# Kernel tuning notes

Hardware: AMD Instinct MI355X
Metric: run time of the kernel (lower is better)

The kernel has to match this reference:

```python
import jax, jax.numpy as jnp
import numpy as np

# hypercfg constants (init_kwargs)
AUX = 0.05
L1W = 5.0
VPW = 1.0
VNW = 1.0


def _lsa_square(cost):
    """Jonker-Volgenant shortest-augmenting-path Hungarian on a square numpy
    cost matrix. Returns rows[j] = row assigned to column j. Runs on host,
    mirroring the original CPU scipy.optimize.linear_sum_assignment call."""
    n = cost.shape[0]
    INF = np.inf
    u = np.zeros(n + 1)
    v = np.zeros(n + 1)
    p = np.zeros(n + 1, dtype=np.int64)   # p[j] = row matched to column j (1-indexed)
    way = np.zeros(n + 1, dtype=np.int64)
    for i in range(1, n + 1):
        p[0] = i
        j0 = 0
        minv = np.full(n + 1, INF)
        used = np.zeros(n + 1, dtype=bool)
        while True:
            used[j0] = True
            i0 = p[j0]
            cur = cost[i0 - 1, :] - u[i0] - v[1:]
            free = ~used[1:]
            upd = free & (cur < minv[1:])
            minv1 = minv[1:]
            minv1[upd] = cur[upd]
            way1 = way[1:]
            way1[upd] = j0
            mfree = np.where(free, minv1, INF)
            j1 = int(np.argmin(mfree)) + 1
            delta = mfree[j1 - 1]
            used_idx = np.nonzero(used)[0]
            u[p[used_idx]] += delta
            v[used_idx] -= delta
            minv1[free] -= delta
            j0 = j1
            if p[j0] == 0:
                break
        while j0 != 0:
            j1 = way[j0]
            p[j0] = p[j1]
            j0 = j1
    return p[1:] - 1


def _match(cost_mk):
    """Rectangular assignment, cost [M, K] with K <= M: pad with a constant
    column block (dummy columns cost the same for any row, so the real K
    columns get the optimal assignment, matching scipy on rectangles)."""
    M, K = cost_mk.shape
    pad = np.zeros((M, M), dtype=np.float64)
    pad[:, :K] = cost_mk
    rows = _lsa_square(pad)
    return rows[:K]


def _cost(meta_points, meta_visibles, gtpoints, gtvisibles):
    # meta_points: [S,B,L,M,2]  gtpoints: [S,B,K,2]
    # meta_visibles: [S,B,M,1]  gtvisibles: [S,B,K,1]
    S, B, L, M, _ = meta_points.shape
    # pairwise L1 cost: [S,B,L,M,K]
    diff = jnp.abs(meta_points[:, :, :, :, None, :] - gtpoints[:, :, None, None, :, :]).sum(-1)
    # delta[l] = L - (l+1), per-layer slack (torch.linspace(1, L, L))
    delta = (L - jnp.arange(1, L + 1, dtype=meta_points.dtype)) * AUX
    cost_p_ml = jax.nn.relu(diff - delta[None, None, :, None, None])
    gtv = gtvisibles[:, :, :, 0][:, :, None, :]          # [S,B,1,K]
    cost_p = gtv * cost_p_ml.mean(2)                     # [S,B,M,K]
    cost_vp = -gtv * jnp.log(meta_visibles)              # [S,B,M,1] -> [S,B,M,K]
    cost_vn = -(1.0 - gtv) * jnp.log(1.0 - meta_visibles)
    cost = L1W * cost_p + VPW * cost_vp + VNW * cost_vn  # [S,B,M,K]
    return cost.mean(0)                                  # mean over shots -> [B,M,K]


def setup_inputs() -> dict:
    key = jax.random.key(0)
    ks = jax.random.split(key, 5)
    S, B, L, M, K = 6, 16, 8, 256, 128
    meta_points = jax.random.uniform(ks[0], (S, B, L, M, 2), dtype=jnp.float32)
    # keep probabilities strictly inside (0,1) so log() is finite
    meta_visibles = jax.random.uniform(ks[1], (S, B, M, 1), dtype=jnp.float32) * 0.9 + 0.05
    covisibles = jax.random.uniform(ks[2], (B, K), dtype=jnp.float32)
    gtpoints = jax.random.uniform(ks[3], (S, B, K, 2), dtype=jnp.float32)
    gtvisibles = (jax.random.uniform(ks[4], (S, B, K, 1)) > 0.5).astype(jnp.float32)
    return {
        "meta_points": meta_points,
        "meta_visibles": meta_visibles,
        "covisibles": covisibles,
        "gtpoints": gtpoints,
        "gtvisibles": gtvisibles,
    }


def reference(meta_points, meta_visibles, covisibles, gtpoints, gtvisibles):
    # covisibles only provides the batch size in the original module
    cost = np.asarray(jax.jit(_cost)(meta_points, meta_visibles, gtpoints, gtvisibles))
    bs = cost.shape[0]
    # per-batch Hungarian on host (sequential data-dependent algorithm);
    # result[b, k] = meta index matched to keypoint k (already kp-sorted,
    # matching the argsort-reorder in the torch code)
    out = np.stack([_match(cost[b]) for b in range(bs)])
    return jnp.asarray(out, dtype=jnp.int64)
```

## Files before the change

kernel.cpp:

```cpp
#include <hip/hip_runtime.h>
#include <math.h>


#define S_ 6
#define B_ 16
#define L_ 8
#define M_ 256
#define K_ 128

__global__ void cost_kernel(const float* __restrict__ mp,
                            const float* __restrict__ mv,
                            const float* __restrict__ gt,
                            const float* __restrict__ gv,
                            float* __restrict__ cost)
{
#pragma clang fp contract(off)
    const int b = blockIdx.x;
    const int m = blockIdx.y;
    const int k = threadIdx.x;

    float accS = 0.0f;
    for (int s = 0; s < S_; ++s) {
        const int sb = s * B_ + b;
        const float gx = gt[(sb * K_ + k) * 2 + 0];
        const float gy = gt[(sb * K_ + k) * 2 + 1];
        float accL = 0.0f;
#pragma unroll
        for (int l = 0; l < L_; ++l) {
            const int base = ((sb * L_ + l) * M_ + m) * 2;
            const float dx = fabsf(mp[base + 0] - gx);
            const float dy = fabsf(mp[base + 1] - gy);
            const float diff = dx + dy;
            const float dl = (float)(L_ - (l + 1)) * 0.05f;
            const float t = diff - dl;
            accL += fmaxf(t, 0.0f);
        }
        const float meanL = accL * 0.125f;
        const float mvv = mv[sb * M_ + m];
        const float gtv = gv[sb * K_ + k];
        const float lp = -logf(mvv);
        const float ln = -logf(1.0f - mvv);
        const float val = (gtv != 0.0f) ? (5.0f * meanL + lp) : ln;
        accS += val;
    }
    cost[(b * M_ + m) * K_ + k] = accS * (1.0f / 6.0f);
}

__device__ __forceinline__ double bits2d(int lo, int hi) {
    const unsigned long long u =
        ((unsigned long long)(unsigned)hi << 32) | (unsigned)lo;
    return __longlong_as_double((long long)u);
}
__device__ __forceinline__ void d2bits(double d, int& lo, int& hi) {
    const unsigned long long u = (unsigned long long)__double_as_longlong(d);
    lo = (int)(u & 0xffffffffull);
    hi = (int)(u >> 32);
}
__device__ __forceinline__ unsigned long long vkey_desc(double v) {
    const double c = v + 0.0;
    const unsigned long long bts = (unsigned long long)__double_as_longlong(c);
    const unsigned long long mask =
        (unsigned long long)((long long)bts >> 63) | 0x8000000000000000ull;
    return ~(bts ^ mask);
}

__global__ __launch_bounds__(64, 1) void match_kernel(const float* __restrict__ cost,
                                                      int* __restrict__ out)
{
#pragma clang fp contract(off)
    const int b = blockIdx.x;
    const int lane = threadIdx.x;
    const float* C = cost + (size_t)b * M_ * K_;
    const double INF = __builtin_inf();
    const int BIG = 0x7fffffff;

    __shared__ float   C_lds[M_ * K_];
    __shared__ double  u_lds[257];
    __shared__ int     p_lds[257];
    __shared__ double  vd_lds[128];
    __shared__ double2 vurec[130];
    __shared__ int     jrec[130];
    __shared__ double  Dcons[128];

    for (int t = lane; t < (M_ * K_) / 4; t += 64)
        ((float4*)C_lds)[t] = ((const float4*)C)[t];

    for (int t = lane; t < 257; t += 64) {
        u_lds[t] = 0.0;
        p_lds[t] = (t >= 129) ? (t - 128) : 0;
    }
    for (int t = lane; t < 128; t += 64) vd_lds[t] = 0.0;
    __syncthreads();

    double v0 = 0.0, v1 = 0.0;

    for (int i = 129; i <= 256; ++i) {
        const int pj0 = p_lds[2 * lane + 1];
        const int pj1 = p_lds[2 * lane + 2];
        float2 cc = *(const float2*)(C_lds + (i - 1) * K_ + 2 * lane);
        const double up0 = u_lds[pj0], up1 = u_lds[pj1];
        double ur0 = up0, ur1 = up1;

        unsigned long long ks0 = vkey_desc(vd_lds[2 * lane]);
        unsigned long long ks1 = vkey_desc(vd_lds[2 * lane + 1]);
        int js0 = 2 * lane + 129;
        int js1 = 2 * lane + 130;
        for (int k = 2; k <= 128; k <<= 1) {
            const bool asc = ((lane & (k >> 1)) == 0);
            for (int d2 = k >> 1; d2 >= 1; d2 >>= 1) {
                if (d2 == 1) {
                    const bool L = (ks0 < ks1) || (ks0 == ks1 && js0 < js1);
                    if (L != asc) {
                        const unsigned long long tk = ks0; ks0 = ks1; ks1 = tk;
                        const int tj = js0; js0 = js1; js1 = tj;
                    }
                } else {
                    const int d = d2 >> 1;
                    const unsigned long long pk0 = __shfl_xor(ks0, d);
                    const int pj0s = __shfl_xor(js0, d);
                    const unsigned long long pk1 = __shfl_xor(ks1, d);
                    const int pj1s = __shfl_xor(js1, d);
                    const bool lower = ((lane & d) == 0);
                    const bool L0 = (ks0 < pk0) || (ks0 == pk0 && js0 < pj0s);
                    const bool L1 = (ks1 < pk1) || (ks1 == pk1 && js1 < pj1s);
                    const bool keep0 = (lower == asc) ? L0 : !L0;
                    const bool keep1 = (lower == asc) ? L1 : !L1;
                    if (!keep0) { ks0 = pk0; js0 = pj0s; }
                    if (!keep1) { ks1 = pk1; js1 = pj1s; }
                }
            }
        }
        jrec[2 * lane] = js0;
        jrec[2 * lane + 1] = js1;
        vurec[2 * lane]     = make_double2(vd_lds[js0 - 129], u_lds[js0 - 128]);
        vurec[2 * lane + 1] = make_double2(vd_lds[js1 - 129], u_lds[js1 - 128]);
        if (lane == 0) { vurec[128] = make_double2(-INF, 0.0); jrec[128] = 257; }
        __syncthreads();

        double2 vuC = vurec[0]; int jdC = jrec[0];
        double2 vuN = vurec[1]; int jdN = jrec[1];
        int ptr = 0;

        int used = 0;
        double u_i0 = 0.0;
        double usum = 0.0;
        int j1 = 0;

        for (;;) {
            const float2 ccs = *(const float2*)(C_lds + (jdC - 129) * K_ + 2 * lane);
            const double dval = (0.0 - u_i0) - vuC.x;

            double cd0 = ((double)cc.x - u_i0) - v0;
            double cd1 = ((double)cc.y - u_i0) - v1;
            if (used & 1) cd0 = INF;
            if (used & 2) cd1 = INF;
            double bv = fmin(cd0, cd1);

            int lo, hi; d2bits(bv, lo, hi);
#define MIN_STAGE(CTRL, RM)                                                      \
            {                                                                    \
                const int nlo = __builtin_amdgcn_update_dpp(lo, lo, CTRL, RM, 0xf, false); \
                const int nhi = __builtin_amdgcn_update_dpp(hi, hi, CTRL, RM, 0xf, false); \
                const double mv2 = fmin(bits2d(lo, hi), bits2d(nlo, nhi));       \
                d2bits(mv2, lo, hi);                                             \
            }
            MIN_STAGE(0x111, 0xf)
            MIN_STAGE(0x112, 0xf)
            MIN_STAGE(0x114, 0xf)
            MIN_STAGE(0x118, 0xf)
            MIN_STAGE(0x142, 0xa)
            MIN_STAGE(0x143, 0xc)
#undef MIN_STAGE
            const int mlo = __builtin_amdgcn_readlane(lo, 63);
            const int mhi = __builtin_amdgcn_readlane(hi, 63);
            const double rmin = bits2d(mlo, mhi);

            if (rmin <= dval) {
                const double delta = rmin;
                usum += delta;
                if (used & 1) { ur0 += delta; v0 -= delta; }
                if (used & 2) { ur1 += delta; v1 -= delta; }

                int jr = BIG;
                if (cd1 == delta) jr = 2 * lane + 2;
                if (cd0 == delta) jr = 2 * lane + 1;
                const unsigned long long br = __ballot(jr != BIG);
                j1 = __builtin_amdgcn_readlane(jr, (int)__builtin_ctzll(br));

                const int ol = (j1 - 1) >> 1, sl = (j1 - 1) & 1;
                const int psel = sl ? pj1 : pj0;
                const int i0n = __builtin_amdgcn_readlane(psel, ol);
                if (i0n == 0) break;

                const double usel = sl ? up1 : up0;
                int ulo, uhi; d2bits(usel, ulo, uhi);
                const double u_n = bits2d(__builtin_amdgcn_readlane(ulo, ol),
                                          __builtin_amdgcn_readlane(uhi, ol));
                if (lane == ol) used |= (1 << sl);
                u_i0 = u_n;
                cc = *(const float2*)(C_lds + (i0n - 1) * K_ + 2 * lane);
            } else {
                const double delta = dval;
                usum += delta;
                if (used & 1) { ur0 += delta; v0 -= delta; }
                if (used & 2) { ur1 += delta; v1 -= delta; }
                if (lane == 0) Dcons[ptr] = usum;
                u_i0 = vuC.y;
                cc = ccs;
                vuC = vuN; jdC = jdN;
                ++ptr;
                vuN = vurec[ptr + 1]; jdN = jrec[ptr + 1];
            }
        }

        __syncthreads();
        if (used & 1) u_lds[pj0] = ur0;
        if (used & 2) u_lds[pj1] = ur1;
        {
            const int t0i = 2 * lane, t1i = 2 * lane + 1;
            if (t0i < ptr) {
                const double amt = usum - Dcons[t0i];
                u_lds[js0 - 128] += amt;
                vd_lds[js0 - 129] -= amt;
            }
            if (t1i < ptr) {
                const double amt = usum - Dcons[t1i];
                u_lds[js1 - 128] += amt;
                vd_lds[js1 - 129] -= amt;
            }
        }
        if (lane == 0) { p_lds[j1] = i; u_lds[i] = usum; }
        __syncthreads();
    }

    for (int j = lane; j < K_; j += 64)
        out[b * K_ + j] = p_lds[j + 1] - 1;
}

extern "C" void kernel_launch(void* const* d_in, const int* in_sizes, int n_in,
                              void* d_out, int out_size, void* d_ws, size_t ws_size,
                              hipStream_t stream) {
    const float* mp = (const float*)d_in[0];
    const float* mv = (const float*)d_in[1];
    const float* gt = (const float*)d_in[3];
    const float* gv = (const float*)d_in[4];
    int* out = (int*)d_out;
    float* cost = (float*)d_ws;

    dim3 gridA(B_, M_);
    cost_kernel<<<gridA, K_, 0, stream>>>(mp, mv, gt, gv, cost);
    match_kernel<<<B_, 64, 0, stream>>>(cost, out);
}
```

Measured before the change: 1.558 ms.

## Cache per-dummy-row column minima and skip runs of dummy-row steps in Hungarian

```diff
diff --git a/kernel.cpp b/kernel.cpp
--- a/kernel.cpp
+++ b/kernel.cpp
@@ -56,6 +56,11 @@
     lo = (int)(u & 0xffffffffull);
     hi = (int)(u >> 32);
 }
+__device__ __forceinline__ double readlane_d(double d, int l) {
+    int lo, hi; d2bits(d, lo, hi);
+    return bits2d(__builtin_amdgcn_readlane(lo, l),
+                  __builtin_amdgcn_readlane(hi, l));
+}
 __device__ __forceinline__ unsigned long long vkey_desc(double v) {
     const double c = v + 0.0;
     const unsigned long long bts = (unsigned long long)__double_as_longlong(c);
@@ -63,6 +68,60 @@
         (unsigned long long)((long long)bts >> 63) | 0x8000000000000000ull;
     return ~(bts ^ mask);
 }
+
+#define RSTG(LOV, HIV, FOP, CTRL, RM)                                            \
+    {                                                                            \
+        const int nlo_ = __builtin_amdgcn_update_dpp(LOV, LOV, CTRL, RM, 0xf, false); \
+        const int nhi_ = __builtin_amdgcn_update_dpp(HIV, HIV, CTRL, RM, 0xf, false); \
+        const double r_ = FOP(bits2d(LOV, HIV), bits2d(nlo_, nhi_));             \
+        d2bits(r_, LOV, HIV);                                                    \
+    }
+#define RLADDER(LOV, HIV, FOP)                                                   \
+    RSTG(LOV, HIV, FOP, 0x111, 0xf)                              \
+    RSTG(LOV, HIV, FOP, 0x112, 0xf)                              \
+    RSTG(LOV, HIV, FOP, 0x114, 0xf)                              \
+    RSTG(LOV, HIV, FOP, 0x118, 0xf)                              \
+    RSTG(LOV, HIV, FOP, 0x142, 0xa)                \
+    RSTG(LOV, HIV, FOP, 0x143, 0xc)
+
+#define FREEMIN(R0B, CMV, CJV)                                                   \
+    {                                                                            \
+        double cd0_ = (double)C_lds[(R0B) * K_ + 2 * lane] - v0;                 \
+        double cd1_ = (double)C_lds[(R0B) * K_ + 2 * lane + 1] - v1;             \
+        if (used & 1) cd0_ = INF;                                                \
+        if (used & 2) cd1_ = INF;                                                \
+        double bv_ = fmin(cd0_, cd1_);                                           \
+        int lo_, hi_; d2bits(bv_, lo_, hi_);                                     \
+        RLADDER(lo_, hi_, fmin)                                                  \
+        CMV = bits2d(__builtin_amdgcn_readlane(lo_, 63),                         \
+                     __builtin_amdgcn_readlane(hi_, 63));                        \
+        int jr_ = BIG;                                                           \
+        if (cd1_ == CMV) jr_ = 2 * lane + 2;                                     \
+        if (cd0_ == CMV) jr_ = 2 * lane + 1;                                     \
+        const unsigned long long br_ = __ballot(jr_ != BIG);                     \
+        CJV = __builtin_amdgcn_readlane(jr_, (int)__builtin_ctzll(br_));         \
+    }
+
+#define SWEEP()                                                                  \
+    {                                                                            \
+        for (int g_ = 0; g_ < 2; ++g_) {                                         \
+            const int R_ = 64 * g_ + lane;                                       \
+            double bm_ = INF; int bc_ = BIG;                                     \
+            for (int it_ = 0; it_ < 128; ++it_) {                                \
+                const int c_ = (it_ + lane) & 127;                               \
+                const double cd_ = (double)C_lds[R_ * K_ + c_] - v_tab[c_];      \
+                if (cd_ < bm_ || (cd_ == bm_ && c_ + 1 < bc_)) {                 \
+                    bm_ = cd_; bc_ = c_ + 1;                                     \
+                }                                                                \
+            }                                                                    \
+            cmin_lds[R_] = bm_; cjmin_lds[R_] = bc_;                             \
+        }                                                                        \
+    }
+
+#define SVREAD(T) readlane_d((((T) & 1) ? sv1 : sv0), (T) >> 1)
+#define SUREAD(T) readlane_d((((T) & 1) ? su1 : su0), (T) >> 1)
+#define DDREAD(T) readlane_d((((T) & 1) ? dd1 : dd0), (T) >> 1)
+#define JSREAD(T) __builtin_amdgcn_readlane(((((T) & 1)) ? js1 : js0), (T) >> 1)
 
 __global__ __launch_bounds__(64, 1) void match_kernel(const float* __restrict__ cost,
                                                       int* __restrict__ out)
@@ -72,24 +131,30 @@
     const int lane = threadIdx.x;
     const float* C = cost + (size_t)b * M_ * K_;
     const double INF = __builtin_inf();
+    const double NINF = -__builtin_inf();
     const int BIG = 0x7fffffff;
 
-    __shared__ float   C_lds[M_ * K_];
-    __shared__ double  u_lds[257];
-    __shared__ int     p_lds[257];
-    __shared__ double  vd_lds[128];
-    __shared__ double2 vurec[130];
-    __shared__ int     jrec[130];
-    __shared__ double  Dcons[128];
+    __shared__ float  C_lds[M_ * K_];
+    __shared__ double u_lds[257];
+    __shared__ int    p_lds[257];
+    __shared__ double vd_lds[128];
+    __shared__ double v_tab[128];
+    __shared__ double cmin_lds[128];
+    __shared__ int    cjmin_lds[128];
+    __shared__ double Sul[128];
+    __shared__ int    Sjl[128];
+    __shared__ double Dcons[128];
 
     for (int t = lane; t < (M_ * K_) / 4; t += 64)
         ((float4*)C_lds)[t] = ((const float4*)C)[t];
-
     for (int t = lane; t < 257; t += 64) {
         u_lds[t] = 0.0;
         p_lds[t] = (t >= 129) ? (t - 128) : 0;
     }
-    for (int t = lane; t < 128; t += 64) vd_lds[t] = 0.0;
+    for (int t = lane; t < 128; t += 64) { vd_lds[t] = 0.0; v_tab[t] = 0.0; }
+    __syncthreads();
+
+    SWEEP()
     __syncthreads();
 
     double v0 = 0.0, v1 = 0.0;
@@ -97,9 +162,7 @@
     for (int i = 129; i <= 256; ++i) {
         const int pj0 = p_lds[2 * lane + 1];
         const int pj1 = p_lds[2 * lane + 2];
-        float2 cc = *(const float2*)(C_lds + (i - 1) * K_ + 2 * lane);
         const double up0 = u_lds[pj0], up1 = u_lds[pj1];
-        double ur0 = up0, ur1 = up1;
 
         unsigned long long ks0 = vkey_desc(vd_lds[2 * lane]);
         unsigned long long ks1 = vkey_desc(vd_lds[2 * lane + 1]);
@@ -109,8 +172,8 @@
             const bool asc = ((lane & (k >> 1)) == 0);
             for (int d2 = k >> 1; d2 >= 1; d2 >>= 1) {
                 if (d2 == 1) {
-                    const bool L = (ks0 < ks1) || (ks0 == ks1 && js0 < js1);
-                    if (L != asc) {
+                    const bool Lc = (ks0 < ks1) || (ks0 == ks1 && js0 < js1);
+                    if (Lc != asc) {
                         const unsigned long long tk = ks0; ks0 = ks1; ks1 = tk;
                         const int tj = js0; js0 = js1; js1 = tj;
                     }
@@ -130,107 +193,120 @@
                 }
             }
         }
-        jrec[2 * lane] = js0;
-        jrec[2 * lane + 1] = js1;
-        vurec[2 * lane]     = make_double2(vd_lds[js0 - 129], u_lds[js0 - 128]);
-        vurec[2 * lane + 1] = make_double2(vd_lds[js1 - 129], u_lds[js1 - 128]);
-        if (lane == 0) { vurec[128] = make_double2(-INF, 0.0); jrec[128] = 257; }
+        const double sv0 = vd_lds[js0 - 129], sv1 = vd_lds[js1 - 129];
+        const double su0 = u_lds[js0 - 128],  su1 = u_lds[js1 - 128];
+        Sul[2 * lane] = su0; Sul[2 * lane + 1] = su1;
+        Sjl[2 * lane] = js0; Sjl[2 * lane + 1] = js1;
         __syncthreads();
 
-        double2 vuC = vurec[0]; int jdC = jrec[0];
-        double2 vuN = vurec[1]; int jdN = jrec[1];
-        int ptr = 0;
-
-        int used = 0;
-        double u_i0 = 0.0;
-        double usum = 0.0;
-        int j1 = 0;
+        const double supm = (lane > 0) ? Sul[2 * lane - 1] : 0.0;
+        const double dd0 = (0.0 - supm) - sv0;
+        const double dd1 = (0.0 - su0) - sv1;
+        const int jprev = (lane > 0) ? Sjl[2 * lane - 1] : 129;
+        const bool f0 = (lane > 0) && (cmin_lds[jprev - 129] <= -sv0);
+        const bool f1 = (cmin_lds[js0 - 129] <= -sv1);
+        const unsigned long long be = __ballot(f0);
+        const unsigned long long bo = __ballot(f1);
+
+        double u = 0.0, usum = 0.0;
+        int used = 0, nU = 0, j1 = 0, ptr = 0;
+        int jU0 = 0, jU1 = 0, jU2 = 0, jU3 = 0;
+        double Ua0 = 0.0, Ua1 = 0.0;
+        int r0b = i - 1;
+        double cm; int cj;
+        FREEMIN(r0b, cm, cj)
 
         for (;;) {
-            const float2 ccs = *(const float2*)(C_lds + (jdC - 129) * K_ + 2 * lane);
-            const double dval = (0.0 - u_i0) - vuC.x;
-
-            double cd0 = ((double)cc.x - u_i0) - v0;
-            double cd1 = ((double)cc.y - u_i0) - v1;
-            if (used & 1) cd0 = INF;
-            if (used & 2) cd1 = INF;
-            double bv = fmin(cd0, cd1);
-
-            int lo, hi; d2bits(bv, lo, hi);
-#define MIN_STAGE(CTRL, RM)                                                      \
-            {                                                                    \
-                const int nlo = __builtin_amdgcn_update_dpp(lo, lo, CTRL, RM, 0xf, false); \
-                const int nhi = __builtin_amdgcn_update_dpp(hi, hi, CTRL, RM, 0xf, false); \
-                const double mv2 = fmin(bits2d(lo, hi), bits2d(nlo, nhi));       \
-                d2bits(mv2, lo, hi);                                             \
+            int tstar;
+            if (ptr >= 128) tstar = 128;
+            else {
+                const double svp = SVREAD(ptr);
+                if (cm <= -svp) tstar = ptr;
+                else {
+                    const int she = (ptr >> 1) + 1;
+                    const int sho = (ptr >> 1) + (ptr & 1);
+                    const unsigned long long mbe =
+                        (she < 64) ? (be & (~0ull << she)) : 0ull;
+                    const unsigned long long mbo =
+                        (sho < 64) ? (bo & (~0ull << sho)) : 0ull;
+                    const int ea = mbe ? 2 * (int)__builtin_ctzll(mbe) : 256;
+                    const int eb = mbo ? 2 * (int)__builtin_ctzll(mbo) + 1 : 256;
+                    tstar = ea < eb ? ea : eb;
+                    if (tstar > 128) tstar = 128;
+                }
             }
-            MIN_STAGE(0x111, 0xf)
-            MIN_STAGE(0x112, 0xf)
-            MIN_STAGE(0x114, 0xf)
-            MIN_STAGE(0x118, 0xf)
-            MIN_STAGE(0x142, 0xa)
-            MIN_STAGE(0x143, 0xc)
-#undef MIN_STAGE
-            const int mlo = __builtin_amdgcn_readlane(lo, 63);
-            const int mhi = __builtin_amdgcn_readlane(hi, 63);
-            const double rmin = bits2d(mlo, mhi);
+            if (tstar > ptr) {
+                const double svp2 = SVREAD(ptr);
+                const double dfirst = (0.0 - u) - svp2;
+                usum = usum + dfirst;
+                if (lane == 0) Dcons[ptr] = usum;
+                for (int k2 = ptr + 1; k2 < tstar; ++k2) {
+                    const double dk = DDREAD(k2);
+                    usum = usum + dk;
+                    if (lane == 0) Dcons[k2] = usum;
+                }
+                u = SUREAD(tstar - 1);
+                r0b = JSREAD(tstar - 1) - 129;
+                ptr = tstar;
+                cm = cmin_lds[r0b]; cj = cjmin_lds[r0b];
+            }
+            const double vh = (ptr < 128) ? SVREAD(ptr) : NINF;
+            const double dval = (0.0 - u) - vh;
+            double rmin; int rj;
+            const bool fastok = (nU < 5) && (cj != jU0) && (cj != jU1)
+                                         && (cj != jU2) && (cj != jU3);
+            if (fastok) { rmin = cm - u; rj = cj; }
+            else { double lm; int lj; FREEMIN(r0b, lm, lj) rmin = lm - u; rj = lj; }
 
             if (rmin <= dval) {
-                const double delta = rmin;
-                usum += delta;
-                if (used & 1) { ur0 += delta; v0 -= delta; }
-                if (used & 2) { ur1 += delta; v1 -= delta; }
-
-                int jr = BIG;
-                if (cd1 == delta) jr = 2 * lane + 2;
-                if (cd0 == delta) jr = 2 * lane + 1;
-                const unsigned long long br = __ballot(jr != BIG);
-                j1 = __builtin_amdgcn_readlane(jr, (int)__builtin_ctzll(br));
-
+                usum = usum + rmin;
+                j1 = rj;
                 const int ol = (j1 - 1) >> 1, sl = (j1 - 1) & 1;
-                const int psel = sl ? pj1 : pj0;
-                const int i0n = __builtin_amdgcn_readlane(psel, ol);
+                const int i0n = __builtin_amdgcn_readlane(sl ? pj1 : pj0, ol);
                 if (i0n == 0) break;
-
-                const double usel = sl ? up1 : up0;
-                int ulo, uhi; d2bits(usel, ulo, uhi);
-                const double u_n = bits2d(__builtin_amdgcn_readlane(ulo, ol),
-                                          __builtin_amdgcn_readlane(uhi, ol));
-                if (lane == ol) used |= (1 << sl);
-                u_i0 = u_n;
-                cc = *(const float2*)(C_lds + (i0n - 1) * K_ + 2 * lane);
+                const double un = readlane_d(sl ? up1 : up0, ol);
+                if (lane == ol) {
+                    used |= (1 << sl);
+                    if (sl == 0) Ua0 = usum; else Ua1 = usum;
+                }
+                if (nU == 0) jU0 = j1; else if (nU == 1) jU1 = j1;
+                else if (nU == 2) jU2 = j1; else if (nU == 3) jU3 = j1;
+                ++nU;
+                u = un;
+                r0b = i0n - 1;
+                FREEMIN(r0b, cm, cj)
             } else {
-                const double delta = dval;
-                usum += delta;
-                if (used & 1) { ur0 += delta; v0 -= delta; }
-                if (used & 2) { ur1 += delta; v1 -= delta; }
+                usum = usum + dval;
                 if (lane == 0) Dcons[ptr] = usum;
-                u_i0 = vuC.y;
-                cc = ccs;
-                vuC = vuN; jdC = jdN;
+                u = SUREAD(ptr);
+                r0b = JSREAD(ptr) - 129;
                 ++ptr;
-                vuN = vurec[ptr + 1]; jdN = jrec[ptr + 1];
+                cm = cmin_lds[r0b]; cj = cjmin_lds[r0b];
             }
         }
 
         __syncthreads();
-        if (used & 1) u_lds[pj0] = ur0;
-        if (used & 2) u_lds[pj1] = ur1;
-        {
-            const int t0i = 2 * lane, t1i = 2 * lane + 1;
-            if (t0i < ptr) {
-                const double amt = usum - Dcons[t0i];
-                u_lds[js0 - 128] += amt;
-                vd_lds[js0 - 129] -= amt;
-            }
-            if (t1i < ptr) {
-                const double amt = usum - Dcons[t1i];
-                u_lds[js1 - 128] += amt;
-                vd_lds[js1 - 129] -= amt;
-            }
+        if (used & 1) { const double a = usum - Ua0; u_lds[pj0] = up0 + a;
+                        v0 -= a; v_tab[2 * lane] = v0; }
+        if (used & 2) { const double a = usum - Ua1; u_lds[pj1] = up1 + a;
+                        v1 -= a; v_tab[2 * lane + 1] = v1; }
+        if (2 * lane < ptr) {
+            const double amt = usum - Dcons[2 * lane];
+            u_lds[js0 - 128] += amt;
+            vd_lds[js0 - 129] -= amt;
+        }
+        if (2 * lane + 1 < ptr) {
+            const double amt = usum - Dcons[2 * lane + 1];
+            u_lds[js1 - 128] += amt;
+            vd_lds[js1 - 129] -= amt;
         }
         if (lane == 0) { p_lds[j1] = i; u_lds[i] = usum; }
         __syncthreads();
+
+        if (nU > 0) {
+            SWEEP()
+            __syncthreads();
+        }
     }
 
     for (int j = lane; j < K_; j += 64)
```

Result: slower. 3.837 ms (+146.3%).
